# Optimization experiments

Measured on AMD Instinct MI355X. Metric: run time of the kernel, lower is better.

Reference implementation:

```python
import jax, jax.numpy as jnp
import numpy as np

D_IN = 1024
D_OUT = 1024
N_HEADS = 16
D_HEAD = D_OUT // N_HEADS


def setup_inputs() -> dict:
    key = jax.random.key(0)
    ks = jax.random.split(key, 6)
    s = 0.02
    return {
        "x": jax.random.normal(ks[0], (4, 2048, D_IN), dtype=jnp.float32),
        "wq": jax.random.normal(ks[1], (D_IN, D_OUT), dtype=jnp.float32) * s,
        "wk": jax.random.normal(ks[2], (D_IN, D_OUT), dtype=jnp.float32) * s,
        "wv": jax.random.normal(ks[3], (D_IN, D_OUT), dtype=jnp.float32) * s,
        "wo": jax.random.normal(ks[4], (D_OUT, D_OUT), dtype=jnp.float32) * s,
        "bo": jax.random.normal(ks[5], (D_OUT,), dtype=jnp.float32) * s,
    }


def reference(x, wq, wk, wv, wo, bo):
    B, T, _ = x.shape
    # QKV projections (no bias), split into heads: (B, H, T, Dh)
    def split_heads(t):
        return t.reshape(B, T, N_HEADS, D_HEAD).transpose(0, 2, 1, 3)
    q = split_heads(x @ wq)
    k = split_heads(x @ wk)
    v = split_heads(x @ wv)
    # attention scores (B, H, T, T), causal mask, scale by sqrt(d_head)
    scores = jnp.einsum("bhqd,bhkd->bhqk", q, k)
    causal = jnp.tril(jnp.ones((T, T), dtype=bool))
    scores = jnp.where(causal, scores, -jnp.inf)
    attn = jax.nn.softmax(scores / jnp.sqrt(jnp.float32(D_HEAD)), axis=-1)
    # dropout = 0.0 (eval) -> identity
    ctx = jnp.einsum("bhqk,bhkd->bhqd", attn, v)
    ctx = ctx.transpose(0, 2, 1, 3).reshape(B, T, D_OUT)
    return ctx @ wo + bo
```

## Files before the change

### kernel.cpp

```cpp
#include <hip/hip_runtime.h>
#include <stdint.h>


typedef unsigned short u16;
typedef __bf16 bf16x8 __attribute__((ext_vector_type(8)));
typedef short s16x4 __attribute__((ext_vector_type(4)));
typedef float f32x4 __attribute__((ext_vector_type(4)));

extern "C" __device__ float __ocml_native_exp2_f32(float);

__device__ __forceinline__ u16 f2bf(float f) {
  union { float f; unsigned u; } v; v.f = f;
  return (u16)((v.u + 0x7fffu + ((v.u >> 16) & 1u)) >> 16);
}

__device__ __forceinline__ void gl_lds16(const void* g, void* l) {
  __builtin_amdgcn_global_load_lds((__attribute__((address_space(1))) void*)g,
                                   (__attribute__((address_space(3))) void*)l,
                                   16, 0, 0);
}

__global__ __launch_bounds__(256) void conv_x_k(const float* __restrict__ x,
                                                u16* __restrict__ xb) {
  int i = (blockIdx.x * 256 + threadIdx.x) * 4;
  float4 v = *reinterpret_cast<const float4*>(x + i);
  ushort4 o;
  o.x = f2bf(v.x); o.y = f2bf(v.y); o.z = f2bf(v.z); o.w = f2bf(v.w);
  *reinterpret_cast<ushort4*>(xb + i) = o;
}

__global__ __launch_bounds__(256) void conv_w_k(const float* __restrict__ w0,
                                                const float* __restrict__ w1,
                                                const float* __restrict__ w2,
                                                const float* __restrict__ w3,
                                                u16* __restrict__ dst) {
  const float* src = blockIdx.z == 0 ? w0 : blockIdx.z == 1 ? w1
                   : blockIdx.z == 2 ? w2 : w3;
  u16* d = dst + (size_t)blockIdx.z * 1024 * 1024;
  __shared__ float tile[32][33];
  int n0 = blockIdx.x * 32, k0 = blockIdx.y * 32;
  int tx = threadIdx.x & 31, ty = threadIdx.x >> 5;
  #pragma unroll
  for (int r = 0; r < 32; r += 8)
    tile[ty + r][tx] = src[(k0 + ty + r) * 1024 + n0 + tx];
  __syncthreads();
  #pragma unroll
  for (int r = 0; r < 32; r += 8)
    d[(n0 + ty + r) * 1024 + k0 + tx] = f2bf(tile[tx][ty + r]);
}

#define SWZ128(row, chunk) ((row) * 128 + ((((chunk) ^ ((row) & 7))) << 4))

__global__ __launch_bounds__(512, 2) void gemm_qkv_k(const u16* __restrict__ A,
                                                     const u16* __restrict__ Wt,
                                                     u16* __restrict__ qw,
                                                     u16* __restrict__ kw,
                                                     u16* __restrict__ vtw) {
  __shared__ u16 SM[49152];
  const int tid = threadIdx.x;
  const int wave = tid >> 6, lane = tid & 63;
  const int quad = lane >> 4, l15 = lane & 15;
  const int m0 = blockIdx.x * 256;
  const int which = blockIdx.y >> 3;
  const int n0 = (blockIdx.y & 7) * 128;
  const u16* Bt = Wt + which * (1024 * 1024);
  const int waveM = (wave >> 1) * 64, waveN = (wave & 1) * 64;

  const f32x4 fz = {0.f, 0.f, 0.f, 0.f};
  f32x4 acc[4][4];
  #pragma unroll
  for (int i = 0; i < 4; i++)
    #pragma unroll
    for (int j = 0; j < 4; j++) acc[i][j] = fz;

  const int lrow8 = lane >> 3, lchunk = lane & 7;
  const int gsw = (lchunk ^ lrow8) * 8;
  const u16* Ag = A + (m0 + wave * 8 + lrow8) * 1024 + gsw;
  const u16* Bg = Bt + (n0 + wave * 8 + lrow8) * 1024 + gsw;

  auto stage = [&](int o, int ktv) {
    #pragma unroll
    for (int i = 0; i < 4; i++)
      gl_lds16(Ag + (i * 64) * 1024 + ktv * 64,
               (char*)SM + o + i * 8192 + wave * 1024);
    #pragma unroll
    for (int i = 0; i < 2; i++)
      gl_lds16(Bg + (i * 64) * 1024 + ktv * 64,
               (char*)SM + o + 32768 + i * 8192 + wave * 1024);
  };

  stage(0, 0);

  for (int s = 0; s < 16; s++) {
    const int o = (s & 1) * 49152;
    __syncthreads();
    if (s < 15) stage(49152 - o, s + 1);

    bf16x8 bfr[4][2];
    #pragma unroll
    for (int nj = 0; nj < 4; nj++)
      #pragma unroll
      for (int kk = 0; kk < 2; kk++)
        bfr[nj][kk] = *reinterpret_cast<const bf16x8*>(
            (char*)SM + o + 32768 + SWZ128(waveN + nj * 16 + l15, kk * 4 + quad));

    bf16x8 af[4][2];
    #pragma unroll
    for (int mi = 0; mi < 4; mi++)
      #pragma unroll
      for (int kk = 0; kk < 2; kk++)
        af[mi][kk] = *reinterpret_cast<const bf16x8*>(
            (char*)SM + o + SWZ128(waveM + mi * 16 + l15, kk * 4 + quad));
    #pragma unroll
    for (int kk = 0; kk < 2; kk++)
      #pragma unroll
      for (int mi = 0; mi < 4; mi++)
        #pragma unroll
        for (int nj = 0; nj < 4; nj++)
          acc[mi][nj] = __builtin_amdgcn_mfma_f32_16x16x32_bf16(
              af[mi][kk], bfr[nj][kk], acc[mi][nj], 0, 0, 0);
  }

  if (which != 2) {
    #pragma unroll
    for (int mi = 0; mi < 4; mi++) {
      #pragma unroll
      for (int r = 0; r < 4; r++) {
        int m = m0 + waveM + mi * 16 + quad * 4 + r;
        int b = m >> 11, t = m & 2047;
        #pragma unroll
        for (int nj = 0; nj < 4; nj++) {
          int n = n0 + waveN + nj * 16 + l15;
          int h = n >> 6, d = n & 63;
          float v = acc[mi][nj][r];
          if (which == 0) qw[((b * 16 + h) * 2048 + t) * 64 + d] = f2bf(v * 0.18033688f);
          else            kw[((b * 16 + h) * 2048 + t) * 64 + d] = f2bf(v);
        }
      }
    }
  } else {
    __syncthreads();
    #pragma unroll
    for (int mi = 0; mi < 4; mi++)
      #pragma unroll
      for (int r = 0; r < 4; r++) {
        int ml = waveM + mi * 16 + quad * 4 + r;
        #pragma unroll
        for (int nj = 0; nj < 4; nj++) {
          int nl = waveN + nj * 16 + l15;
          int byte = nl * 512 + ((((ml >> 3) ^ (nl & 7))) << 4) + (ml & 7) * 2;
          *(u16*)((char*)SM + byte) = f2bf(acc[mi][nj][r]);
        }
      }
    __syncthreads();
    const int b = m0 >> 11, t0 = m0 & 2047;
    #pragma unroll
    for (int i = 0; i < 8; i++) {
      int cid = tid + 512 * i;
      int nl = cid >> 5, tc = cid & 31;
      int jb = tc >> 3, cp = tc & 7;
      int gl = ((2 * cp) & 3) * 4 + ((2 * cp) >> 2);
      int gh = ((2 * cp + 1) & 3) * 4 + ((2 * cp + 1) >> 2);
      int ml0 = jb * 64 + gl * 4, ml1 = jb * 64 + gh * 4;
      s16x4 lo = *reinterpret_cast<const s16x4*>(
          (char*)SM + nl * 512 + (((ml0 >> 3) ^ (nl & 7)) << 4) + (ml0 & 7) * 2);
      s16x4 hi = *reinterpret_cast<const s16x4*>(
          (char*)SM + nl * 512 + (((ml1 >> 3) ^ (nl & 7)) << 4) + (ml1 & 7) * 2);
      union { s16x4 hh[2]; bf16x8 w; } uu;
      uu.hh[0] = lo; uu.hh[1] = hi;
      int n = n0 + nl;
      int h = n >> 6, d = n & 63;
      *reinterpret_cast<bf16x8*>(
          vtw + (((size_t)(b * 16 + h) * 64 + d) * 2048 + t0 + tc * 8)) = uu.w;
    }
  }
}

__global__ __launch_bounds__(256) void attn_k(const u16* __restrict__ Q,
                                              const u16* __restrict__ K,
                                              const u16* __restrict__ Vt,
                                              u16* __restrict__ ctx) {
  __shared__ u16 Qs[64 * 64];
  __shared__ u16 Ks[2][64 * 64];
  __shared__ u16 Vs[2][64 * 64];
  const int tid = threadIdx.x;
  const int wave = tid >> 6, lane = tid & 63;
  const int quad = lane >> 4, l15 = lane & 15;
  const int bh = blockIdx.x;
  const int qt = 31 - (int)blockIdx.y;
  const int b = bh >> 4, h = bh & 15;

  const u16* Qg = Q + (bh * 2048 + qt * 64) * 64;
  const u16* Kg = K + bh * (2048 * 64);
  const u16* Vg = Vt + bh * (64 * 2048);

  const int lrow = tid >> 3;
  const int lsw = ((tid & 7) ^ (lrow & 7)) * 8;

  gl_lds16(Qg + lrow * 64 + lsw, (char*)Qs + wave * 1024);
  gl_lds16(Qg + (32 + lrow) * 64 + lsw, (char*)Qs + wave * 1024 + 4096);
  {
    char* KsB = (char*)Ks[0] + wave * 1024;
    char* VsB = (char*)Vs[0] + wave * 1024;
    gl_lds16(Kg + lrow * 64 + lsw, KsB);
    gl_lds16(Kg + (32 + lrow) * 64 + lsw, KsB + 4096);
    gl_lds16(Vg + lrow * 2048 + lsw, VsB);
    gl_lds16(Vg + (32 + lrow) * 2048 + lsw, VsB + 4096);
  }

  const s16x4 ones4 = {(short)0x3F80, (short)0x3F80, (short)0x3F80, (short)0x3F80};
  const f32x4 fz = {0.f, 0.f, 0.f, 0.f};
  f32x4 accO[4];
  f32x4 accL = fz;
  #pragma unroll
  for (int dt = 0; dt < 4; dt++) accO[dt] = fz;
  bf16x8 qf[2];

  #define SWZB(row, chunk) ((row) * 128 + (((chunk) ^ ((row) & 7)) << 4))

  for (int j = 0; j <= qt; j++) {
    const int cur = j & 1;
    __syncthreads();
    if (j < qt) {
      char* KsB = (char*)Ks[cur ^ 1] + wave * 1024;
      char* VsB = (char*)Vs[cur ^ 1] + wave * 1024;
      const int jr = (j + 1) * 64;
      gl_lds16(Kg + (jr + lrow) * 64 + lsw, KsB);
      gl_lds16(Kg + (jr + 32 + lrow) * 64 + lsw, KsB + 4096);
      gl_lds16(Vg + lrow * 2048 + jr + lsw, VsB);
      gl_lds16(Vg + (32 + lrow) * 2048 + jr + lsw, VsB + 4096);
    }
    if (j == 0) {
      #pragma unroll
      for (int kk = 0; kk < 2; kk++)
        qf[kk] = *reinterpret_cast<const bf16x8*>(
            (char*)Qs + SWZB(wave * 16 + l15, kk * 4 + quad));
    }

    f32x4 s[4];
    #pragma unroll
    for (int nt = 0; nt < 4; nt++) s[nt] = fz;
    #pragma unroll
    for (int kk = 0; kk < 2; kk++)
      #pragma unroll
      for (int nt = 0; nt < 4; nt++) {
        bf16x8 kf = *reinterpret_cast<const bf16x8*>(
            (char*)Ks[cur] + SWZB(nt * 16 + l15, kk * 4 + quad));
        s[nt] = __builtin_amdgcn_mfma_f32_16x16x32_bf16(kf, qf[kk], s[nt], 0, 0, 0);
      }

    if (j == qt) {
      const int qrow = wave * 16 + l15;
      #pragma unroll
      for (int nt = 0; nt < 4; nt++)
        #pragma unroll
        for (int r = 0; r < 4; r++)
          if (nt * 16 + quad * 4 + r > qrow) s[nt][r] = -1e30f;
    }

    s16x4 pf[4];
    #pragma unroll
    for (int nt = 0; nt < 4; nt++) {
      float p0 = __ocml_native_exp2_f32(s[nt][0]);
      float p1 = __ocml_native_exp2_f32(s[nt][1]);
      float p2 = __ocml_native_exp2_f32(s[nt][2]);
      float p3 = __ocml_native_exp2_f32(s[nt][3]);
      union { s16x4 v; unsigned u[2]; } pk;
      pk.u[0] = __builtin_amdgcn_perm(__float_as_uint(p1), __float_as_uint(p0),
                                      0x07060302u);
      pk.u[1] = __builtin_amdgcn_perm(__float_as_uint(p3), __float_as_uint(p2),
                                      0x07060302u);
      pf[nt] = pk.v;
    }

    union { bf16x8 w; s16x4 hh[2]; } vv[2][4];
    #pragma unroll
    for (int r2 = 0; r2 < 2; r2++)
      #pragma unroll
      for (int dt = 0; dt < 4; dt++) {
        int row = dt * 16 + l15;
        vv[r2][dt].w = *reinterpret_cast<const bf16x8*>(
            (char*)Vs[cur] + row * 128 + (((quad * 2 + r2) ^ (row & 7)) << 4));
      }
    #pragma unroll
    for (int kc = 0; kc < 4; kc++) {
      accL = __builtin_amdgcn_mfma_f32_16x16x16bf16_1k(pf[kc], ones4, accL, 0, 0, 0);
      #pragma unroll
      for (int dt = 0; dt < 4; dt++)
        accO[dt] = __builtin_amdgcn_mfma_f32_16x16x16bf16_1k(
            pf[kc], vv[kc >> 1][dt].hh[kc & 1], accO[dt], 0, 0, 0);
    }
  }
  #undef SWZB

  float inv[4];
  #pragma unroll
  for (int r = 0; r < 4; r++) inv[r] = 1.0f / accL[r];
  const int trow = qt * 64 + wave * 16 + quad * 4;
  #pragma unroll
  for (int dt = 0; dt < 4; dt++)
    #pragma unroll
    for (int r = 0; r < 4; r++)
      ctx[(b * 2048 + trow + r) * 1024 + h * 64 + dt * 16 + l15] =
          f2bf(accO[dt][r] * inv[r]);
}

__global__ __launch_bounds__(256) void gemm_out_k(const u16* __restrict__ A,
                                                  const u16* __restrict__ Wt,
                                                  const float* __restrict__ bo,
                                                  float* __restrict__ out) {
  __shared__ u16 SM[32768];
  const int tid = threadIdx.x;
  const int wave = tid >> 6, lane = tid & 63;
  const int quad = lane >> 4, l15 = lane & 15;
  const int m0 = blockIdx.x * 128;
  const int n0 = blockIdx.y * 128;
  const int waveM = (wave >> 1) * 64, waveN = (wave & 1) * 64;

  const f32x4 fz = {0.f, 0.f, 0.f, 0.f};
  f32x4 acc[4][4];
  #pragma unroll
  for (int i = 0; i < 4; i++)
    #pragma unroll
    for (int j = 0; j < 4; j++) acc[i][j] = fz;

  const int lrow8 = lane >> 3, lchunk = lane & 7;
  const int gsw = (lchunk ^ lrow8) * 8;
  const u16* Agp[4];
  const u16* Bgp[4];
  #pragma unroll
  for (int i = 0; i < 4; i++) {
    Agp[i] = A + (m0 + i * 32 + wave * 8 + lrow8) * 1024 + gsw;
    Bgp[i] = Wt + (n0 + i * 32 + wave * 8 + lrow8) * 1024 + gsw;
  }

  #pragma unroll
  for (int i = 0; i < 4; i++) {
    gl_lds16(Agp[i], (char*)SM + i * 4096 + wave * 1024);
    gl_lds16(Bgp[i], (char*)SM + 32768 + i * 4096 + wave * 1024);
  }

  #pragma unroll
  for (int s = 0; s < 16; s++) {
    const int o = (s & 1) * 16384;
    __syncthreads();
    if (s < 15) {
      const int nxt = 16384 - o;
      const int koff = (s + 1) * 64;
      #pragma unroll
      for (int i = 0; i < 4; i++) {
        gl_lds16(Agp[i] + koff, (char*)SM + nxt + i * 4096 + wave * 1024);
        gl_lds16(Bgp[i] + koff, (char*)SM + 32768 + nxt + i * 4096 + wave * 1024);
      }
    }
    #pragma unroll
    for (int kk = 0; kk < 2; kk++) {
      bf16x8 af[4], bf[4];
      #pragma unroll
      for (int mi = 0; mi < 4; mi++)
        af[mi] = *reinterpret_cast<const bf16x8*>(
            (char*)SM + o + SWZ128(waveM + mi * 16 + l15, kk * 4 + quad));
      #pragma unroll
      for (int ni = 0; ni < 4; ni++)
        bf[ni] = *reinterpret_cast<const bf16x8*>(
            (char*)SM + 32768 + o + SWZ128(waveN + ni * 16 + l15, kk * 4 + quad));
      #pragma unroll
      for (int mi = 0; mi < 4; mi++)
        #pragma unroll
        for (int ni = 0; ni < 4; ni++)
          acc[mi][ni] = __builtin_amdgcn_mfma_f32_16x16x32_bf16(af[mi], bf[ni], acc[mi][ni], 0, 0, 0);
    }
  }
  float bias[4];
  #pragma unroll
  for (int ni = 0; ni < 4; ni++) bias[ni] = bo[n0 + waveN + ni * 16 + l15];
  #pragma unroll
  for (int mi = 0; mi < 4; mi++)
    #pragma unroll
    for (int r = 0; r < 4; r++) {
      int m = m0 + waveM + mi * 16 + quad * 4 + r;
      #pragma unroll
      for (int ni = 0; ni < 4; ni++) {
        int n = n0 + waveN + ni * 16 + l15;
        out[(size_t)m * 1024 + n] = acc[mi][ni][r] + bias[ni];
      }
    }
}

extern "C" void kernel_launch(void* const* d_in, const int* in_sizes, int n_in,
                              void* d_out, int out_size, void* d_ws, size_t ws_size,
                              hipStream_t stream) {
  const float* x  = (const float*)d_in[0];
  const float* wq = (const float*)d_in[1];
  const float* wk = (const float*)d_in[2];
  const float* wv = (const float*)d_in[3];
  const float* wo = (const float*)d_in[4];
  const float* bo = (const float*)d_in[5];
  float* out = (float*)d_out;
  char* ws = (char*)d_ws;

  u16* xb  = (u16*)(ws);
  u16* wt  = (u16*)(ws + 16777216);
  u16* qw  = (u16*)(ws + 25165824);
  u16* kw  = (u16*)(ws + 41943040);
  u16* vtw = (u16*)(ws + 58720256);

  conv_x_k<<<8192, 256, 0, stream>>>(x, xb);
  conv_w_k<<<dim3(32, 32, 4), 256, 0, stream>>>(wq, wk, wv, wo, wt);
  gemm_qkv_k<<<dim3(32, 24), 512, 0, stream>>>(xb, wt, qw, kw, vtw);
  attn_k<<<dim3(64, 32), 256, 0, stream>>>(qw, kw, vtw, xb );
  gemm_out_k<<<dim3(64, 8), 256, 0, stream>>>(xb, wt + 3 * 1024 * 1024, bo, out);
}
```

Measured before the change: 231.6 us.

## Process two 64-row query tiles per attention block to reuse K/V tiles

Each attention workgroup now handles 128 query rows, split into two 64-row sub-tiles, instead of 64. Every K/V tile loaded into shared memory is used by both sub-tiles, which halves K/V global traffic and barriers per unit of query work. The first sub-tile skips the last K block, and the diagonal mask is applied separately for each. The cost is twice the accumulator registers, which may lower occupancy, and half as many workgroups (1024), with causal imbalance between them.

```diff
diff --git a/kernel.cpp b/kernel.cpp
--- a/kernel.cpp
+++ b/kernel.cpp
@@ -180,25 +180,27 @@
                                               const u16* __restrict__ K,
                                               const u16* __restrict__ Vt,
                                               u16* __restrict__ ctx) {
-  __shared__ u16 Qs[64 * 64];
+  __shared__ u16 Qs[128 * 64];
   __shared__ u16 Ks[2][64 * 64];
   __shared__ u16 Vs[2][64 * 64];
   const int tid = threadIdx.x;
   const int wave = tid >> 6, lane = tid & 63;
   const int quad = lane >> 4, l15 = lane & 15;
   const int bh = blockIdx.x;
-  const int qt = 31 - (int)blockIdx.y;
+  const int qt = 15 - (int)blockIdx.y;
   const int b = bh >> 4, h = bh & 15;
 
-  const u16* Qg = Q + (bh * 2048 + qt * 64) * 64;
+  const u16* Qg = Q + (bh * 2048 + qt * 128) * 64;
   const u16* Kg = K + bh * (2048 * 64);
   const u16* Vg = Vt + bh * (64 * 2048);
 
   const int lrow = tid >> 3;
   const int lsw = ((tid & 7) ^ (lrow & 7)) * 8;
 
-  gl_lds16(Qg + lrow * 64 + lsw, (char*)Qs + wave * 1024);
-  gl_lds16(Qg + (32 + lrow) * 64 + lsw, (char*)Qs + wave * 1024 + 4096);
+  #pragma unroll
+  for (int c = 0; c < 4; c++)
+    gl_lds16(Qg + (c * 32 + lrow) * 64 + lsw,
+             (char*)Qs + c * 4096 + wave * 1024);
   {
     char* KsB = (char*)Ks[0] + wave * 1024;
     char* VsB = (char*)Vs[0] + wave * 1024;
@@ -210,18 +212,25 @@
 
   const s16x4 ones4 = {(short)0x3F80, (short)0x3F80, (short)0x3F80, (short)0x3F80};
   const f32x4 fz = {0.f, 0.f, 0.f, 0.f};
-  f32x4 accO[4];
-  f32x4 accL = fz;
-  #pragma unroll
-  for (int dt = 0; dt < 4; dt++) accO[dt] = fz;
-  bf16x8 qf[2];
+  f32x4 accO[2][4];
+  f32x4 accL[2];
+  #pragma unroll
+  for (int u = 0; u < 2; u++) {
+    accL[u] = fz;
+    #pragma unroll
+    for (int dt = 0; dt < 4; dt++) accO[u][dt] = fz;
+  }
+  bf16x8 qf[2][2];
 
   #define SWZB(row, chunk) ((row) * 128 + (((chunk) ^ ((row) & 7)) << 4))
 
-  for (int j = 0; j <= qt; j++) {
+  const int jdiag0 = 2 * qt;
+  const int jmax = 2 * qt + 1;
+
+  for (int j = 0; j <= jmax; j++) {
     const int cur = j & 1;
     __syncthreads();
-    if (j < qt) {
+    if (j < jmax) {
       char* KsB = (char*)Ks[cur ^ 1] + wave * 1024;
       char* VsB = (char*)Vs[cur ^ 1] + wave * 1024;
       const int jr = (j + 1) * 64;
@@ -232,45 +241,71 @@
     }
     if (j == 0) {
       #pragma unroll
-      for (int kk = 0; kk < 2; kk++)
-        qf[kk] = *reinterpret_cast<const bf16x8*>(
-            (char*)Qs + SWZB(wave * 16 + l15, kk * 4 + quad));
-    }
-
-    f32x4 s[4];
-    #pragma unroll
-    for (int nt = 0; nt < 4; nt++) s[nt] = fz;
+      for (int u = 0; u < 2; u++)
+        #pragma unroll
+        for (int kk = 0; kk < 2; kk++)
+          qf[u][kk] = *reinterpret_cast<const bf16x8*>(
+              (char*)Qs + SWZB(u * 64 + wave * 16 + l15, kk * 4 + quad));
+    }
+
+    f32x4 s0[4], s1[4];
+    #pragma unroll
+    for (int nt = 0; nt < 4; nt++) { s0[nt] = fz; s1[nt] = fz; }
     #pragma unroll
     for (int kk = 0; kk < 2; kk++)
       #pragma unroll
       for (int nt = 0; nt < 4; nt++) {
         bf16x8 kf = *reinterpret_cast<const bf16x8*>(
             (char*)Ks[cur] + SWZB(nt * 16 + l15, kk * 4 + quad));
-        s[nt] = __builtin_amdgcn_mfma_f32_16x16x32_bf16(kf, qf[kk], s[nt], 0, 0, 0);
-      }
-
-    if (j == qt) {
-      const int qrow = wave * 16 + l15;
+        if (j <= jdiag0)
+          s0[nt] = __builtin_amdgcn_mfma_f32_16x16x32_bf16(kf, qf[0][kk], s0[nt], 0, 0, 0);
+        s1[nt] = __builtin_amdgcn_mfma_f32_16x16x32_bf16(kf, qf[1][kk], s1[nt], 0, 0, 0);
+      }
+
+    const int qrow = wave * 16 + l15;
+    if (j == jdiag0) {
       #pragma unroll
       for (int nt = 0; nt < 4; nt++)
         #pragma unroll
         for (int r = 0; r < 4; r++)
-          if (nt * 16 + quad * 4 + r > qrow) s[nt][r] = -1e30f;
-    }
-
-    s16x4 pf[4];
+          if (nt * 16 + quad * 4 + r > qrow) s0[nt][r] = -1e30f;
+    }
+    if (j == jmax) {
+      #pragma unroll
+      for (int nt = 0; nt < 4; nt++)
+        #pragma unroll
+        for (int r = 0; r < 4; r++)
+          if (nt * 16 + quad * 4 + r > qrow) s1[nt][r] = -1e30f;
+    }
+
+    s16x4 pf0[4], pf1[4];
+    if (j <= jdiag0) {
+      #pragma unroll
+      for (int nt = 0; nt < 4; nt++) {
+        float p0 = __ocml_native_exp2_f32(s0[nt][0]);
+        float p1 = __ocml_native_exp2_f32(s0[nt][1]);
+        float p2 = __ocml_native_exp2_f32(s0[nt][2]);
+        float p3 = __ocml_native_exp2_f32(s0[nt][3]);
+        union { s16x4 v; unsigned u[2]; } pk;
+        pk.u[0] = __builtin_amdgcn_perm(__float_as_uint(p1), __float_as_uint(p0),
+                                        0x07060302u);
+        pk.u[1] = __builtin_amdgcn_perm(__float_as_uint(p3), __float_as_uint(p2),
+                                        0x07060302u);
+        pf0[nt] = pk.v;
+      }
+    }
     #pragma unroll
     for (int nt = 0; nt < 4; nt++) {
-      float p0 = __ocml_native_exp2_f32(s[nt][0]);
-      float p1 = __ocml_native_exp2_f32(s[nt][1]);
-      float p2 = __ocml_native_exp2_f32(s[nt][2]);
-      float p3 = __ocml_native_exp2_f32(s[nt][3]);
+      float p0 = __ocml_native_exp2_f32(s1[nt][0]);
+      float p1 = __ocml_native_exp2_f32(s1[nt][1]);
+      float p2 = __ocml_native_exp2_f32(s1[nt][2]);
+      float p3 = __ocml_native_exp2_f32(s1[nt][3]);
       union { s16x4 v; unsigned u[2]; } pk;
       pk.u[0] = __builtin_amdgcn_perm(__float_as_uint(p1), __float_as_uint(p0),
                                       0x07060302u);
       pk.u[1] = __builtin_amdgcn_perm(__float_as_uint(p3), __float_as_uint(p2),
                                       0x07060302u);
-      pf[nt] = pk.v;
+      pf1[nt] = pk.v;
     }
 
     union { bf16x8 w; s16x4 hh[2]; } vv[2][4];
@@ -284,25 +319,35 @@
       }
     #pragma unroll
     for (int kc = 0; kc < 4; kc++) {
-      accL = __builtin_amdgcn_mfma_f32_16x16x16bf16_1k(pf[kc], ones4, accL, 0, 0, 0);
+      if (j <= jdiag0) {
+        accL[0] = __builtin_amdgcn_mfma_f32_16x16x16bf16_1k(pf0[kc], ones4, accL[0], 0, 0, 0);
+        #pragma unroll
+        for (int dt = 0; dt < 4; dt++)
+          accO[0][dt] = __builtin_amdgcn_mfma_f32_16x16x16bf16_1k(
+              pf0[kc], vv[kc >> 1][dt].hh[kc & 1], accO[0][dt], 0, 0, 0);
+      }
+      accL[1] = __builtin_amdgcn_mfma_f32_16x16x16bf16_1k(pf1[kc], ones4, accL[1], 0, 0, 0);
       #pragma unroll
       for (int dt = 0; dt < 4; dt++)
-        accO[dt] = __builtin_amdgcn_mfma_f32_16x16x16bf16_1k(
-            pf[kc], vv[kc >> 1][dt].hh[kc & 1], accO[dt], 0, 0, 0);
+        accO[1][dt] = __builtin_amdgcn_mfma_f32_16x16x16bf16_1k(
+            pf1[kc], vv[kc >> 1][dt].hh[kc & 1], accO[1][dt], 0, 0, 0);
     }
   }
   #undef SWZB
 
-  float inv[4];
-  #pragma unroll
-  for (int r = 0; r < 4; r++) inv[r] = 1.0f / accL[r];
-  const int trow = qt * 64 + wave * 16 + quad * 4;
-  #pragma unroll
-  for (int dt = 0; dt < 4; dt++)
-    #pragma unroll
-    for (int r = 0; r < 4; r++)
-      ctx[(b * 2048 + trow + r) * 1024 + h * 64 + dt * 16 + l15] =
-          f2bf(accO[dt][r] * inv[r]);
+  #pragma unroll
+  for (int u = 0; u < 2; u++) {
+    float inv[4];
+    #pragma unroll
+    for (int r = 0; r < 4; r++) inv[r] = 1.0f / accL[u][r];
+    const int trow = qt * 128 + u * 64 + wave * 16 + quad * 4;
+    #pragma unroll
+    for (int dt = 0; dt < 4; dt++)
+      #pragma unroll
+      for (int r = 0; r < 4; r++)
+        ctx[(b * 2048 + trow + r) * 1024 + h * 64 + dt * 16 + l15] =
+            f2bf(accO[u][dt][r] * inv[r]);
+  }
 }
 
 __global__ __launch_bounds__(256) void gemm_out_k(const u16* __restrict__ A,
@@ -408,6 +453,6 @@
   conv_x_k<<<8192, 256, 0, stream>>>(x, xb);
   conv_w_k<<<dim3(32, 32, 4), 256, 0, stream>>>(wq, wk, wv, wo, wt);
   gemm_qkv_k<<<dim3(32, 24), 512, 0, stream>>>(xb, wt, qw, kw, vtw);
-  attn_k<<<dim3(64, 32), 256, 0, stream>>>(qw, kw, vtw, xb );
+  attn_k<<<dim3(64, 16), 256, 0, stream>>>(qw, kw, vtw, xb );
   gemm_out_k<<<dim3(64, 8), 256, 0, stream>>>(xb, wt + 3 * 1024 * 1024, bo, out);
 }
```

After: 254.4 us. 1.1x slower.
